# Kernel tuning notes

Measured on AMD Instinct MI355X. Metric: run time of the kernel, lower is better.

The kernel has to match this reference:

```python
import jax, jax.numpy as jnp
import numpy as np

GAMMA = 1.0

def setup_inputs() -> dict:
    key = jax.random.key(0)
    k1, k2 = jax.random.split(key)
    source_features = jax.random.normal(k1, (4096, 2048), dtype=jnp.float32)
    target_features = jax.random.normal(k2, (4096, 2048), dtype=jnp.float32)
    return {"source_features": source_features, "target_features": target_features}

def _gaussian_kernel_mean(x, y, gamma):
    # Original: ((x_i - y_j)**2).mean(-1) / D  == sqdist_ij / D**2
    # Computed via the x^2 + y^2 - 2xy GEMM trick instead of tiling O(N*M*D).
    d = x.shape[1]
    x2 = jnp.sum(x * x, axis=1)  # [N]
    y2 = jnp.sum(y * y, axis=1)  # [M]
    xy = x @ y.T                 # [N, M]
    sqdist = x2[:, None] + y2[None, :] - 2.0 * xy
    k = jnp.exp(-gamma * sqdist / (d * d))
    return jnp.mean(k)

def reference(source_features, target_features):
    source = source_features.reshape(source_features.shape[0], -1)
    target = target_features.reshape(target_features.shape[0], -1)
    # Equal batch sizes -> padding branch in the original is a no-op.
    xx = _gaussian_kernel_mean(source, source, GAMMA)
    yy = _gaussian_kernel_mean(target, target, GAMMA)
    xy = _gaussian_kernel_mean(source, target, GAMMA)
    return xx + yy - 2.0 * xy
```

## Files before the change

kernel.cpp:

```cpp
#include <hip/hip_runtime.h>
#include <stdint.h>
#include <stddef.h>

#define AS1 __attribute__((address_space(1)))
#define AS3 __attribute__((address_space(3)))

typedef short bf16x8 __attribute__((ext_vector_type(8)));
typedef float f32x4 __attribute__((ext_vector_type(4)));
typedef unsigned short u16x8 __attribute__((ext_vector_type(8)));

static constexpr int N = 4096;
static constexpr int K = 2048;
static constexpr int BM = 128;
static constexpr int TILES = N / BM;
static constexpr int NBLK = TILES * TILES;

__device__ __forceinline__ unsigned short f2bf(float f) {
  union { float f; uint32_t u; } v; v.f = f;
  return (unsigned short)((v.u + 0x7FFFu + ((v.u >> 16) & 1u)) >> 16);
}

__global__ __launch_bounds__(256) void prep_kernel(
    const float* __restrict__ X, const float* __restrict__ Y,
    float* __restrict__ x2, float* __restrict__ y2,
    unsigned short* __restrict__ Xb, unsigned short* __restrict__ Yb, int wb) {
  const int row = blockIdx.x;
  const float* src = blockIdx.y ? Y : X;
  float* nrm = blockIdx.y ? y2 : x2;
  unsigned short* dst = blockIdx.y ? Yb : Xb;
  const size_t base = (size_t)row * K + threadIdx.x * 8;
  const float4 a = *(const float4*)(src + base);
  const float4 b = *(const float4*)(src + base + 4);
  double s = (double)a.x * a.x + (double)a.y * a.y + (double)a.z * a.z +
             (double)a.w * a.w + (double)b.x * b.x + (double)b.y * b.y +
             (double)b.z * b.z + (double)b.w * b.w;
  if (wb) {
    u16x8 o;
    o[0] = f2bf(a.x); o[1] = f2bf(a.y); o[2] = f2bf(a.z); o[3] = f2bf(a.w);
    o[4] = f2bf(b.x); o[5] = f2bf(b.y); o[6] = f2bf(b.z); o[7] = f2bf(b.w);
    *(u16x8*)(dst + base) = o;
  }
#pragma unroll
  for (int off = 32; off; off >>= 1) s += __shfl_down(s, off);
  __shared__ double red[4];
  if ((threadIdx.x & 63) == 0) red[threadIdx.x >> 6] = s;
  __syncthreads();
  if (threadIdx.x == 0) nrm[row] = (float)(red[0] + red[1] + red[2] + red[3]);
}


#define RB(bb, o, ks) ((unsigned)((bb)*32768u + (o)*16384u + (ks)*8192u))
#define VM10 asm volatile("s_waitcnt vmcnt(10)" ::: "memory")
#define VM_NONE

#define STAGE(O, KS, TT, BB)                                                   \
  do {                                                                         \
    const unsigned short* _sp = (O) ? Bpan : Apan;                             \
    const unsigned int _kof = (unsigned)(TT) * 64u + (KS) * 32u;               \
    const unsigned int _lb = RB(BB, O, KS) + wseg;                             \
    __builtin_amdgcn_global_load_lds(                                          \
        (const AS1 unsigned int*)(_sp + ((O) ? sB0 : sA0) + _kof),             \
        (AS3 unsigned int*)(lds + _lb), 16, 0, 0);                             \
    __builtin_amdgcn_global_load_lds(                                          \
        (const AS1 unsigned int*)(_sp + ((O) ? sB1 : sA1) + _kof),             \
        (AS3 unsigned int*)(lds + _lb + 512u), 16, 0, 0);                      \
  } while (0)

#define PHASE(KS, NH, BB, VMW, ...)                                            \
  do {                                                                         \
    if constexpr ((NH) == 0) {                                                 \
      _Pragma("unroll") for (int _mi = 0; _mi < 8; ++_mi)                      \
          af[_mi] = *(const bf16x8*)(lds + RB(BB, 0, KS) + aoff[_mi]);         \
    }                                                                          \
    bf16x8 _b0 = *(const bf16x8*)(lds + RB(BB, 1, KS) + boff[(NH) * 2]);       \
    bf16x8 _b1 = *(const bf16x8*)(lds + RB(BB, 1, KS) + boff[(NH) * 2 + 1]);   \
    __VA_ARGS__;                                                               \
    __builtin_amdgcn_s_barrier();                                              \
    __builtin_amdgcn_s_setprio(1);                                             \
    _Pragma("unroll") for (int _mi = 0; _mi < 8; ++_mi) {                      \
      acc[_mi][(NH) * 2] = __builtin_amdgcn_mfma_f32_16x16x32_bf16(            \
          af[_mi], _b0, acc[_mi][(NH) * 2], 0, 0, 0);                          \
      acc[_mi][(NH) * 2 + 1] = __builtin_amdgcn_mfma_f32_16x16x32_bf16(        \
          af[_mi], _b1, acc[_mi][(NH) * 2 + 1], 0, 0, 0);                      \
    }                                                                          \
    __builtin_amdgcn_s_setprio(0);                                             \
    VMW;                                                                       \
    __builtin_amdgcn_s_barrier();                                              \
  } while (0)

#define TILE(T, BB)                                                            \
  do {                                                                         \
    const int _t1 = ((T) + 1 < 32) ? (T) + 1 : 31;                             \
    const int _t2 = ((T) + 2 < 32) ? (T) + 2 : 31;                             \
    PHASE(0, 0, BB, VM_NONE, STAGE(1, 1, _t1, 1 - (BB)));                      \
    PHASE(0, 1, BB, VM10, STAGE(0, 0, _t2, BB));                               \
    PHASE(1, 0, BB, VM_NONE, STAGE(1, 0, _t2, BB));                            \
    PHASE(1, 1, BB, VM10, STAGE(0, 1, _t2, BB));                               \
  } while (0)

__global__ __launch_bounds__(512, 2) void mmd_gemm8(
    const unsigned short* __restrict__ Xb, const unsigned short* __restrict__ Yb,
    const float* __restrict__ x2, const float* __restrict__ y2,
    double* __restrict__ partials) {
  __shared__ __align__(16) unsigned short lds[65536];

  const int bid = blockIdx.x;
  const int logical = (bid & 7) * 62 + (bid >> 3);
  int ti, tj;
  const unsigned short *Apan, *Bpan;
  const float *rn, *cn;
  double wgt;
  if (logical < 256) {
    ti = logical & 15; tj = logical >> 4;
    Apan = Xb; Bpan = Yb; rn = x2; cn = y2; wgt = -2.0;
  } else {
    const int q = logical - 256;
    const int pp = q / 120;
    int jj = q % 120;
    int rr = 0;
    while (jj >= 15 - rr) { jj -= 15 - rr; ++rr; }
    ti = rr; tj = rr + 1 + jj;
    Apan = Bpan = pp ? Yb : Xb;
    rn = cn = pp ? y2 : x2;
    wgt = 2.0;
  }
  const int i0 = ti << 8, j0 = tj << 8;

  const int tid = threadIdx.x;
  const int w = tid >> 6, l = tid & 63;
  const int wm = w >> 2, wn = w & 3;
  const int lr = l & 15, lq = l >> 4;

  const int ci0 = w * 128 + l;
  const int ci1 = ci0 + 64;
  const int r0 = ci0 >> 2, r1 = ci1 >> 2;
  const int c0 = ((ci0 & 3) - (r0 >> 2)) & 3;
  const int c1 = ((ci1 & 3) - (r1 >> 2)) & 3;
  const unsigned int sA0 = (unsigned)(i0 + r0) * (unsigned)K + (unsigned)(c0 * 8);
  const unsigned int sA1 = (unsigned)(i0 + r1) * (unsigned)K + (unsigned)(c1 * 8);
  const unsigned int sB0 = (unsigned)(j0 + r0) * (unsigned)K + (unsigned)(c0 * 8);
  const unsigned int sB1 = (unsigned)(j0 + r1) * (unsigned)K + (unsigned)(c1 * 8);
  const unsigned int wseg = (unsigned)w * 1024u;

  unsigned int aoff[8], boff[4];
#pragma unroll
  for (int mi = 0; mi < 8; ++mi) {
    const int r = wm * 128 + mi * 16 + lr;
    aoff[mi] = (unsigned)(r * 32 + (((lq + (r >> 2)) & 3) * 8));
  }
#pragma unroll
  for (int ni = 0; ni < 4; ++ni) {
    const int rb = wn * 64 + ni * 16 + lr;
    boff[ni] = (unsigned)(rb * 32 + (((lq + (rb >> 2)) & 3) * 8));
  }

  f32x4 acc[8][4] = {};
  bf16x8 af[8];

  STAGE(0, 0, 0, 0); STAGE(1, 0, 0, 0); STAGE(0, 1, 0, 0); STAGE(1, 1, 0, 0);
  STAGE(0, 0, 1, 1); STAGE(1, 0, 1, 1); STAGE(0, 1, 1, 1);
  VM10;
  __builtin_amdgcn_s_barrier();

#pragma unroll 1
  for (int tt = 0; tt < 32; tt += 2) {
    TILE(tt, 0);
    TILE(tt + 1, 1);
  }

  const float ce = -1.0f / (2048.0f * 2048.0f);
  double s = 0.0;
#pragma unroll
  for (int mi = 0; mi < 8; ++mi) {
#pragma unroll
    for (int r4 = 0; r4 < 4; ++r4) {
      const float rv = rn[i0 + wm * 128 + mi * 16 + lq * 4 + r4];
#pragma unroll
      for (int ni = 0; ni < 4; ++ni) {
        const float cv = cn[j0 + wn * 64 + ni * 16 + lr];
        const float tx = ce * (rv + cv - 2.0f * acc[mi][ni][r4]);
        const float v =
            tx * (1.0f + tx * (0.5f + tx * (0.16666667f + tx * 0.041666668f)));
        s += (double)v;
      }
    }
  }
#pragma unroll
  for (int off = 32; off; off >>= 1) s += __shfl_down(s, off);
  __shared__ double red[8];
  if (l == 0) red[w] = s;
  __syncthreads();
  if (tid == 0) {
    double tot = 0.0;
#pragma unroll
    for (int i = 0; i < 8; ++i) tot += red[i];
    partials[logical] = wgt * tot;
  }
}

__global__ __launch_bounds__(256) void mmd_sym128(
    const unsigned short* __restrict__ Xb, const unsigned short* __restrict__ Yb,
    const float* __restrict__ x2, const float* __restrict__ y2,
    double* __restrict__ partials) {
  const int bid = blockIdx.x;
  const int logical = (bid & 7) * 12 + (bid >> 3);
  const int p = logical / 48;
  const int r2_ = logical % 48;
  const int d = r2_ / 3;
  const int sub = r2_ % 3;
  const double wgt = (sub == 1) ? 2.0 : 1.0;

  const unsigned short* Pan = p ? Yb : Xb;
  const float* nrm = p ? y2 : x2;
  const int i0 = d * 256 + ((sub == 2) ? 128 : 0);
  const int j0 = d * 256 + ((sub >= 1) ? 128 : 0);

  __shared__ __align__(16) unsigned short As[128 * 64];
  __shared__ __align__(16) unsigned short Bs[128 * 64];

  const int tid = threadIdx.x;
  const int w = tid >> 6, l = tid & 63;
  const int m_base = (w >> 1) * 64, n_base = (w & 1) * 64;
  const int lr = l & 15, lq = l >> 4;

  f32x4 acc[4][4] = {};

  for (int k0 = 0; k0 < K; k0 += 64) {
#pragma unroll
    for (int u = 0; u < 4; ++u) {
      const int seg = w * 4 + u;
      const int f = seg * 64 + l;
      const int row = f >> 3;
      const int scol = ((f & 7) ^ (row & 7)) * 8;
      __builtin_amdgcn_global_load_lds(
          (const AS1 unsigned int*)(Pan + (size_t)(i0 + row) * K + k0 + scol),
          (AS3 unsigned int*)(As + seg * 512), 16, 0, 0);
      __builtin_amdgcn_global_load_lds(
          (const AS1 unsigned int*)(Pan + (size_t)(j0 + row) * K + k0 + scol),
          (AS3 unsigned int*)(Bs + seg * 512), 16, 0, 0);
    }
    __syncthreads();

#pragma unroll
    for (int kk = 0; kk < 64; kk += 32) {
      bf16x8 af2[4], bfr[4];
      const int ch = (kk >> 3) + lq;
#pragma unroll
      for (int mi = 0; mi < 4; ++mi) {
        const int r = m_base + mi * 16 + lr;
        af2[mi] = *(const bf16x8*)((const char*)As + r * 128 + ((ch ^ (r & 7)) * 16));
      }
#pragma unroll
      for (int ni = 0; ni < 4; ++ni) {
        const int r = n_base + ni * 16 + lr;
        bfr[ni] = *(const bf16x8*)((const char*)Bs + r * 128 + ((ch ^ (r & 7)) * 16));
      }
#pragma unroll
      for (int mi = 0; mi < 4; ++mi)
#pragma unroll
        for (int ni = 0; ni < 4; ++ni)
          acc[mi][ni] = __builtin_amdgcn_mfma_f32_16x16x32_bf16(
              af2[mi], bfr[ni], acc[mi][ni], 0, 0, 0);
    }
    __syncthreads();
  }

  const float ce = -1.0f / (2048.0f * 2048.0f);
  double s = 0.0;
#pragma unroll
  for (int mi = 0; mi < 4; ++mi) {
#pragma unroll
    for (int r4 = 0; r4 < 4; ++r4) {
      const float rv = nrm[i0 + m_base + mi * 16 + lq * 4 + r4];
#pragma unroll
      for (int ni = 0; ni < 4; ++ni) {
        const float cv = nrm[j0 + n_base + ni * 16 + lr];
        const float tx = ce * (rv + cv - 2.0f * acc[mi][ni][r4]);
        const float v =
            tx * (1.0f + tx * (0.5f + tx * (0.16666667f + tx * 0.041666668f)));
        s += (double)v;
      }
    }
  }
#pragma unroll
  for (int off = 32; off; off >>= 1) s += __shfl_down(s, off);
  __shared__ double red[4];
  if (l == 0) red[w] = s;
  __syncthreads();
  if (tid == 0)
    partials[496 + logical] = wgt * (red[0] + red[1] + red[2] + red[3]);
}

__global__ __launch_bounds__(256) void mmd_gemm_f32(
    const float* __restrict__ Xp, const float* __restrict__ Yp,
    const float* __restrict__ x2, const float* __restrict__ y2,
    double* __restrict__ partials) {
  const int p = blockIdx.y;
  const float* Ap = (p == 1) ? Yp : Xp;
  const float* Bp = (p == 0) ? Xp : Yp;
  const float* rn = (p == 1) ? y2 : x2;
  const float* cn = (p == 0) ? x2 : y2;
  const double wgt = (p == 2) ? -2.0 : 1.0;

  const int bx = blockIdx.x;
  const int i0 = (bx & (TILES - 1)) * BM;
  const int j0 = (bx / TILES) * BM;

  __shared__ __align__(16) unsigned short As[BM * 64];
  __shared__ __align__(16) unsigned short Bs[BM * 64];

  const int tid = threadIdx.x;
  const int w = tid >> 6, l = tid & 63;
  const int m_base = (w >> 1) * 64, n_base = (w & 1) * 64;

  f32x4 acc[4][4] = {};

  for (int k0 = 0; k0 < K; k0 += 64) {
#pragma unroll
    for (int u = 0; u < 4; ++u) {
      const int f = u * 256 + tid;
      const int row = f >> 3;
      const int cir = f & 7;
      const int dstb = row * 128 + ((cir ^ (row & 7)) * 16);
      {
        const float* g = Ap + (size_t)(i0 + row) * K + k0 + cir * 8;
        const float4 v0 = *(const float4*)g;
        const float4 v1 = *(const float4*)(g + 4);
        u16x8 o;
        o[0] = f2bf(v0.x); o[1] = f2bf(v0.y); o[2] = f2bf(v0.z); o[3] = f2bf(v0.w);
        o[4] = f2bf(v1.x); o[5] = f2bf(v1.y); o[6] = f2bf(v1.z); o[7] = f2bf(v1.w);
        *(u16x8*)((char*)As + dstb) = o;
      }
      {
        const float* g = Bp + (size_t)(j0 + row) * K + k0 + cir * 8;
        const float4 v0 = *(const float4*)g;
        const float4 v1 = *(const float4*)(g + 4);
        u16x8 o;
        o[0] = f2bf(v0.x); o[1] = f2bf(v0.y); o[2] = f2bf(v0.z); o[3] = f2bf(v0.w);
        o[4] = f2bf(v1.x); o[5] = f2bf(v1.y); o[6] = f2bf(v1.z); o[7] = f2bf(v1.w);
        *(u16x8*)((char*)Bs + dstb) = o;
      }
    }
    __syncthreads();

#pragma unroll
    for (int kk = 0; kk < 64; kk += 32) {
      bf16x8 af2[4], bfr[4];
      const int lr = l & 15;
      const int ch = (kk >> 3) + (l >> 4);
#pragma unroll
      for (int mi = 0; mi < 4; ++mi) {
        const int r = m_base + mi * 16 + lr;
        af2[mi] = *(const bf16x8*)((const char*)As + r * 128 + ((ch ^ (r & 7)) * 16));
      }
#pragma unroll
      for (int ni = 0; ni < 4; ++ni) {
        const int r = n_base + ni * 16 + lr;
        bfr[ni] = *(const bf16x8*)((const char*)Bs + r * 128 + ((ch ^ (r & 7)) * 16));
      }
#pragma unroll
      for (int mi = 0; mi < 4; ++mi)
#pragma unroll
        for (int ni = 0; ni < 4; ++ni)
          acc[mi][ni] = __builtin_amdgcn_mfma_f32_16x16x32_bf16(
              af2[mi], bfr[ni], acc[mi][ni], 0, 0, 0);
    }
    __syncthreads();
  }

  const float ce = -1.0f / (2048.0f * 2048.0f);
  double s = 0.0;
  const int lr = l & 15, lq = l >> 4;
#pragma unroll
  for (int mi = 0; mi < 4; ++mi) {
#pragma unroll
    for (int r4 = 0; r4 < 4; ++r4) {
      const float rv = rn[i0 + m_base + mi * 16 + lq * 4 + r4];
#pragma unroll
      for (int ni = 0; ni < 4; ++ni) {
        const float cv = cn[j0 + n_base + ni * 16 + lr];
        const float tx = ce * (rv + cv - 2.0f * acc[mi][ni][r4]);
        const float v =
            tx * (1.0f + tx * (0.5f + tx * (0.16666667f + tx * 0.041666668f)));
        s += (double)v;
      }
    }
  }
#pragma unroll
  for (int off = 32; off; off >>= 1) s += __shfl_down(s, off);
  __shared__ double red[4];
  if (l == 0) red[w] = s;
  __syncthreads();
  if (tid == 0) partials[p * NBLK + bx] = wgt * (red[0] + red[1] + red[2] + red[3]);
}

__global__ __launch_bounds__(256) void finalize_kernel(
    const double* __restrict__ partials, float* __restrict__ out, int n) {
  double s = 0.0;
  for (int i = threadIdx.x; i < n; i += 256) s += partials[i];
#pragma unroll
  for (int off = 32; off; off >>= 1) s += __shfl_down(s, off);
  __shared__ double red[4];
  if ((threadIdx.x & 63) == 0) red[threadIdx.x >> 6] = s;
  __syncthreads();
  if (threadIdx.x == 0)
    out[0] = (float)((red[0] + red[1] + red[2] + red[3]) *
                     (1.0 / ((double)N * (double)N)));
}

extern "C" void kernel_launch(void* const* d_in, const int* in_sizes, int n_in,
                              void* d_out, int out_size, void* d_ws,
                              size_t ws_size, hipStream_t stream) {
  const float* X = (const float*)d_in[0];
  const float* Y = (const float*)d_in[1];
  char* ws = (char*)d_ws;

  double* partials = (double*)ws;
  float* x2 = (float*)(ws + 24576);
  float* y2 = (float*)(ws + 24576 + 16384);
  unsigned short* Xb = (unsigned short*)(ws + 65536);
  unsigned short* Yb = Xb + (size_t)N * K;
  const size_t need_fast = (size_t)65536 + (size_t)2 * N * K * 2;
  const bool fast = ws_size >= need_fast;

  prep_kernel<<<dim3(N, 2), 256, 0, stream>>>(X, Y, x2, y2, Xb, Yb, fast ? 1 : 0);
  if (fast) {
    mmd_gemm8<<<dim3(496), dim3(512), 0, stream>>>(Xb, Yb, x2, y2, partials);
    mmd_sym128<<<dim3(96), dim3(256), 0, stream>>>(Xb, Yb, x2, y2, partials);
    finalize_kernel<<<1, 256, 0, stream>>>(partials, (float*)d_out, 592);
  } else {
    mmd_gemm_f32<<<dim3(NBLK, 3), 256, 0, stream>>>(X, Y, x2, y2, partials);
    finalize_kernel<<<1, 256, 0, stream>>>(partials, (float*)d_out, 3072);
  }
}
```

Measured before the change: 183.0 us.

## Restage LDS tiles as 64-wide rows with XOR swizzle and shallower prefetch

Changes the shared-memory layout from two 32-element K-slices per operand into a single 64-element-wide row per tile row, using an XOR swizzle keyed on row to avoid bank conflicts. Each global-to-LDS load now covers contiguous 128-byte row segments, and the half-tile split moves from the K dimension to the row dimension. The prefetch schedule is rewritten so that the next tile is mostly staged within the current tile and the wait count drops from 10 to 2 outstanding loads. This is meant to improve global load coalescing and LDS read efficiency, at the cost of less load-in-flight depth, which may expose memory latency.

Result: no change. 180.1 us (-1.6%).

```diff
diff --git a/kernel.cpp b/kernel.cpp
--- a/kernel.cpp
+++ b/kernel.cpp
@@ -49,31 +49,35 @@
 }
 
 
-#define RB(bb, o, ks) ((unsigned)((bb)*32768u + (o)*16384u + (ks)*8192u))
-#define VM10 asm volatile("s_waitcnt vmcnt(10)" ::: "memory")
+#define RB3(bb, o) ((unsigned)((bb)*32768u + (o)*16384u))
+#define VM2 asm volatile("s_waitcnt vmcnt(2)" ::: "memory")
 #define VM_NONE
 
-#define STAGE(O, KS, TT, BB)                                                   \
+#define STG(O, TT, BB, H)                                                      \
   do {                                                                         \
     const unsigned short* _sp = (O) ? Bpan : Apan;                             \
-    const unsigned int _kof = (unsigned)(TT) * 64u + (KS) * 32u;               \
-    const unsigned int _lb = RB(BB, O, KS) + wseg;                             \
+    const unsigned int _so =                                                   \
+        ((O) ? sB : sA) + (unsigned)(H) * 262144u + (unsigned)(TT) * 64u;      \
+    const unsigned int _lb = RB3(BB, O) + (unsigned)(H) * 8192u + wseg;        \
     __builtin_amdgcn_global_load_lds(                                          \
-        (const AS1 unsigned int*)(_sp + ((O) ? sB0 : sA0) + _kof),             \
+        (const AS1 unsigned int*)(_sp + _so),                                  \
         (AS3 unsigned int*)(lds + _lb), 16, 0, 0);                             \
     __builtin_amdgcn_global_load_lds(                                          \
-        (const AS1 unsigned int*)(_sp + ((O) ? sB1 : sA1) + _kof),             \
+        (const AS1 unsigned int*)(_sp + _so + 16384u),                         \
         (AS3 unsigned int*)(lds + _lb + 512u), 16, 0, 0);                      \
   } while (0)
 
-#define PHASE(KS, NH, BB, VMW, ...)                                            \
+#define PH(KS, NH, BB, VMW, ...)                                               \
   do {                                                                         \
     if constexpr ((NH) == 0) {                                                 \
       _Pragma("unroll") for (int _mi = 0; _mi < 8; ++_mi)                      \
-          af[_mi] = *(const bf16x8*)(lds + RB(BB, 0, KS) + aoff[_mi]);         \
+          af[_mi] = *(const bf16x8*)(lds + RB3(BB, 0) +                        \
+                                     (aoff[_mi] ^ ((KS) * 32u)));              \
     }                                                                          \
-    bf16x8 _b0 = *(const bf16x8*)(lds + RB(BB, 1, KS) + boff[(NH) * 2]);       \
-    bf16x8 _b1 = *(const bf16x8*)(lds + RB(BB, 1, KS) + boff[(NH) * 2 + 1]);   \
+    bf16x8 _b0 = *(const bf16x8*)(lds + RB3(BB, 1) +                           \
+                                  (boff[(NH) * 2] ^ ((KS) * 32u)));            \
+    bf16x8 _b1 = *(const bf16x8*)(lds + RB3(BB, 1) +                           \
+                                  (boff[(NH) * 2 + 1] ^ ((KS) * 32u)));        \
     __VA_ARGS__;                                                               \
     __builtin_amdgcn_s_barrier();                                              \
     __builtin_amdgcn_s_setprio(1);                                             \
@@ -88,14 +92,14 @@
     __builtin_amdgcn_s_barrier();                                              \
   } while (0)
 
-#define TILE(T, BB)                                                            \
+#define TILE3(T, BB)                                                           \
   do {                                                                         \
     const int _t1 = ((T) + 1 < 32) ? (T) + 1 : 31;                             \
     const int _t2 = ((T) + 2 < 32) ? (T) + 2 : 31;                             \
-    PHASE(0, 0, BB, VM_NONE, STAGE(1, 1, _t1, 1 - (BB)));                      \
-    PHASE(0, 1, BB, VM10, STAGE(0, 0, _t2, BB));                               \
-    PHASE(1, 0, BB, VM_NONE, STAGE(1, 0, _t2, BB));                            \
-    PHASE(1, 1, BB, VM10, STAGE(0, 1, _t2, BB));                               \
+    PH(0, 0, BB, VM_NONE, STG(0, _t1, 1 - (BB), 1));                           \
+    PH(0, 1, BB, VM_NONE, STG(1, _t1, 1 - (BB), 0));                           \
+    PH(1, 0, BB, VM_NONE, STG(1, _t1, 1 - (BB), 1));                           \
+    PH(1, 1, BB, VM2,     STG(0, _t2, (BB), 0));                               \
   } while (0)
 
 __global__ __launch_bounds__(512, 2) void mmd_gemm8(
@@ -131,41 +135,37 @@
   const int wm = w >> 2, wn = w & 3;
   const int lr = l & 15, lq = l >> 4;
 
-  const int ci0 = w * 128 + l;
-  const int ci1 = ci0 + 64;
-  const int r0 = ci0 >> 2, r1 = ci1 >> 2;
-  const int c0 = ((ci0 & 3) - (r0 >> 2)) & 3;
-  const int c1 = ((ci1 & 3) - (r1 >> 2)) & 3;
-  const unsigned int sA0 = (unsigned)(i0 + r0) * (unsigned)K + (unsigned)(c0 * 8);
-  const unsigned int sA1 = (unsigned)(i0 + r1) * (unsigned)K + (unsigned)(c1 * 8);
-  const unsigned int sB0 = (unsigned)(j0 + r0) * (unsigned)K + (unsigned)(c0 * 8);
-  const unsigned int sB1 = (unsigned)(j0 + r1) * (unsigned)K + (unsigned)(c1 * 8);
+  const int ci = w * 128 + l;
+  const int rr0 = ci >> 3;
+  const int cc0 = (ci & 7) ^ (rr0 & 7);
+  const unsigned int sA = (unsigned)(i0 + rr0) * (unsigned)K + (unsigned)(cc0 * 8);
+  const unsigned int sB = (unsigned)(j0 + rr0) * (unsigned)K + (unsigned)(cc0 * 8);
   const unsigned int wseg = (unsigned)w * 1024u;
 
   unsigned int aoff[8], boff[4];
 #pragma unroll
   for (int mi = 0; mi < 8; ++mi) {
     const int r = wm * 128 + mi * 16 + lr;
-    aoff[mi] = (unsigned)(r * 32 + (((lq + (r >> 2)) & 3) * 8));
+    aoff[mi] = (unsigned)(r * 64 + ((lq ^ (r & 7)) * 8));
   }
 #pragma unroll
   for (int ni = 0; ni < 4; ++ni) {
     const int rb = wn * 64 + ni * 16 + lr;
-    boff[ni] = (unsigned)(rb * 32 + (((lq + (rb >> 2)) & 3) * 8));
+    boff[ni] = (unsigned)(rb * 64 + ((lq ^ (rb & 7)) * 8));
   }
 
   f32x4 acc[8][4] = {};
   bf16x8 af[8];
 
-  STAGE(0, 0, 0, 0); STAGE(1, 0, 0, 0); STAGE(0, 1, 0, 0); STAGE(1, 1, 0, 0);
-  STAGE(0, 0, 1, 1); STAGE(1, 0, 1, 1); STAGE(0, 1, 1, 1);
-  VM10;
+  STG(0, 0, 0, 0); STG(0, 0, 0, 1); STG(1, 0, 0, 0); STG(1, 0, 0, 1);
+  STG(0, 1, 1, 0);
+  VM2;
   __builtin_amdgcn_s_barrier();
 
 #pragma unroll 1
   for (int tt = 0; tt < 32; tt += 2) {
-    TILE(tt, 0);
-    TILE(tt + 1, 1);
+    TILE3(tt, 0);
+    TILE3(tt + 1, 1);
   }
 
   const float ce = -1.0f / (2048.0f * 2048.0f);
```
